# Kernel tuning notes

Measured on AMD Instinct MI355X. Metric: run time of the kernel, lower is better.

Reference implementation:

```python
import jax, jax.numpy as jnp
import numpy as np

B, L, D, H = 2, 2048, 2048, 16
DH = D // H  # 128 per-head dim
EPS = 1e-5


def setup_inputs() -> dict:
    key = jax.random.key(0)
    ks = jax.random.split(key, 6)
    s = 0.02  # xavier-ish init scale with gain 2**-2.5
    return {
        "hidden_states": jax.random.normal(ks[0], (B, L, D), jnp.float32),
        "Wq": jax.random.normal(ks[1], (D, D), jnp.float32) * s,
        "Wk": jax.random.normal(ks[2], (D, D), jnp.float32) * s,
        "Wv": jax.random.normal(ks[3], (D, D), jnp.float32) * s,
        "Wb": jax.random.normal(ks[4], (D, H), jnp.float32) * s,
        "o_norm_weight": jnp.ones((DH,), jnp.float32),
        "Wo": jax.random.normal(ks[5], (D, D), jnp.float32) * s,
    }


def _delta_rule(q, k, v, beta):
    """Recurrent delta-rule linear attention.
    q,k,v: [B,H,L,Dh]; beta: [B,H,L]. Math identical to fused_chunk_delta_rule.
    S_t = S_{t-1} + k_t (beta_t * (v_t - S_{t-1}^T k_t))^T ;  o_t = S_t^T q_t
    """
    def step(S, inp):
        qt, kt, vt, bt = inp  # [B,H,Dh],[B,H,Dh],[B,H,Dh],[B,H]
        v_pred = jnp.einsum('bhk,bhkv->bhv', kt, S)
        delta = (vt - v_pred) * bt[..., None]
        S = S + kt[..., None] * delta[:, :, None, :]
        ot = jnp.einsum('bhk,bhkv->bhv', qt, S)
        return S, ot

    xs = (q.transpose(2, 0, 1, 3), k.transpose(2, 0, 1, 3),
          v.transpose(2, 0, 1, 3), beta.transpose(2, 0, 1))
    S0 = jnp.zeros(q.shape[:2] + (q.shape[-1], v.shape[-1]), q.dtype)
    _, o = jax.lax.scan(step, S0, xs)  # o: [L,B,H,Dh]
    return o.transpose(1, 2, 0, 3)  # [B,H,L,Dh]


def reference(hidden_states, Wq, Wk, Wv, Wb, o_norm_weight, Wo):
    b, l, d = hidden_states.shape
    h = Wb.shape[1]
    dh = d // h

    q = hidden_states @ Wq
    k = hidden_states @ Wk
    v = jax.nn.silu(hidden_states @ Wv)

    def heads(x):
        return x.reshape(b, l, h, dh).transpose(0, 2, 1, 3)  # b h l d

    q, k, v = heads(q), heads(k), heads(v)

    # qk_norm = 'l2' (torch F.normalize with eps clamp)
    def l2n(x):
        n = jnp.sqrt(jnp.sum(x * x, axis=-1, keepdims=True))
        return x / jnp.maximum(n, 1e-12)

    q, k = l2n(q), l2n(k)
    q = q * (dh ** -0.5)  # fla delta-rule default scale

    beta = jax.nn.sigmoid(hidden_states @ Wb).transpose(0, 2, 1)  # b h l

    o = _delta_rule(q, k, v, beta)  # b h l dh
    o = o.transpose(0, 2, 1, 3)  # b l h dh

    # RMSNorm over head_v_dim
    o = o * jax.lax.rsqrt(jnp.mean(o * o, axis=-1, keepdims=True) + EPS)
    o = o * o_norm_weight

    return o.reshape(b, l, d) @ Wo
```

## Files before the change

kernel.cpp:

```cpp
#include <hip/hip_runtime.h>
#include <hip/hip_bf16.h>
#include <cstdint>

#define DEV static __device__ __forceinline__

typedef unsigned short u16;
typedef unsigned int u32;
typedef __attribute__((ext_vector_type(8))) short short8;
typedef __attribute__((ext_vector_type(4))) float f32x4;

constexpr int Bn = 2, Ln = 2048, Dn = 2048, Hn = 16;
constexpr int Mrows = Bn * Ln;
constexpr int CHK = 64, NCK = Ln / CHK;
constexpr int NCHUNKS = Bn * Hn * NCK;

DEV float b2f(u16 s) { union { float f; u32 u; } x; x.u = ((u32)s) << 16; return x.f; }
DEV u16 f2b(float f) {
  union { float f; u32 u; } x; x.f = f; u32 u = x.u;
  return (u16)((u + 0x7fffu + ((u >> 16) & 1u)) >> 16);
}

DEV void cp16(const void* g, void* l) {
  __builtin_amdgcn_global_load_lds(
      (const __attribute__((address_space(1))) u32*)(unsigned long long)(g),
      (__attribute__((address_space(3))) u32*)(unsigned long long)(l), 16, 0, 0);
}

DEV f32x4 mfma16(short8 a, short8 b, f32x4 c) {
  return __builtin_amdgcn_mfma_f32_16x16x32_bf16(a, b, c, 0, 0, 0);
}

__global__ void k_cvt(const float* __restrict__ src, u16* __restrict__ dst, int n8) {
  int i = blockIdx.x * blockDim.x + threadIdx.x;
  if (i >= n8) return;
  const float4* s4 = (const float4*)(src + (size_t)i * 8);
  float4 a = s4[0], b = s4[1];
  u16 o[8] = {f2b(a.x), f2b(a.y), f2b(a.z), f2b(a.w), f2b(b.x), f2b(b.y), f2b(b.z), f2b(b.w)};
  *(short8*)(dst + (size_t)i * 8) = *(short8*)o;
}

struct TransArgs {
  const float* src[5]; u16* dst[5]; int rows[5]; int cols[5];
};
__global__ void k_trans(TransArgs t) {
  __shared__ u16 tile[32][33];
  int z = blockIdx.z;
  const float* src = t.src[z]; u16* dst = t.dst[z];
  int rows = t.rows[z], cols = t.cols[z];
  int r0 = blockIdx.y * 32, c0 = blockIdx.x * 32;
  if (r0 >= rows || c0 >= cols) return;
  int tx = threadIdx.x, ty = threadIdx.y;
  for (int i = ty; i < 32; i += 8) {
    int r = r0 + i, c = c0 + tx;
    if (r < rows && c < cols) tile[i][tx] = f2b(src[(size_t)r * cols + c]);
  }
  __syncthreads();
  for (int i = ty; i < 32; i += 8) {
    int r = c0 + i, c = r0 + tx;
    if (r < cols && c < rows) dst[(size_t)r * rows + c] = tile[tx][i];
  }
}

__global__ __launch_bounds__(256) void k_beta(const u16* __restrict__ hs,
                                              const u16* __restrict__ WbT,
                                              float* __restrict__ beta_g) {
  __shared__ float part[256];
  int tid = threadIdx.x, wave = tid >> 6, lane = tid & 63, quad = lane >> 4, l15 = lane & 15;
  int tok0 = blockIdx.x * 16;
  const u16* arow = hs + (size_t)(tok0 + l15) * Dn + wave * 512;
  const u16* brow = WbT + (size_t)l15 * Dn + wave * 512;
  f32x4 acc = {0.f, 0.f, 0.f, 0.f};
#pragma unroll
  for (int k = 0; k < 512; k += 32) {
    short8 af = *(const short8*)&arow[k + quad * 8];
    short8 bf = *(const short8*)&brow[k + quad * 8];
    acc = mfma16(af, bf, acc);
  }
  part[tid] = 0.f;
  __syncthreads();
#pragma unroll
  for (int r = 0; r < 4; r++) atomicAdd(&part[l15 * 16 + quad * 4 + r], acc[r]);
  __syncthreads();
  int h = tid >> 4, tr = tid & 15;
  int b = tok0 >> 11;
  int l = (tok0 + tr) & 2047;
  beta_g[(size_t)(b * Hn + h) * Ln + l] = 1.f / (1.f + __expf(-part[h * 16 + tr]));
}

struct GemmArgs {
  const u16* A; const u16* Bt; void* C; int epi;
  int f32out;
  int M, N, K;
};
__global__ __launch_bounds__(256) void k_gemm(GemmArgs g) {
  __shared__ u16 As[128 * 64];
  __shared__ u16 Bs[128 * 64];
  const u16* A = g.A; const u16* Bt = g.Bt;
  int epi = g.epi;
  int K = g.K, N = g.N;
  int tid = threadIdx.x, wave = tid >> 6, lane = tid & 63;
  int quad = lane >> 4, l15 = lane & 15;
  int lin = blockIdx.y * gridDim.x + blockIdx.x;
  int cpx = (gridDim.x * gridDim.y) >> 3;
  int wg2 = (lin & 7) * cpx + (lin >> 3);
  int bx2 = wg2 % gridDim.x, by2 = wg2 / gridDim.x;
  int m0 = by2 * 128, n0 = bx2 * 128;
  int wm = (wave >> 1) * 64, wn = (wave & 1) * 64;
  f32x4 acc[4][4];
#pragma unroll
  for (int i = 0; i < 4; i++)
#pragma unroll
    for (int j = 0; j < 4; j++) acc[i][j] = (f32x4){0.f, 0.f, 0.f, 0.f};
  int scol = ((lane & 7) ^ (lane >> 3)) * 8;
  const u16* Ag = A + (size_t)(m0 + wave * 32 + (lane >> 3)) * K + scol;
  const u16* Bg = Bt + (size_t)(n0 + wave * 32 + (lane >> 3)) * K + scol;
  u16* Al = &As[wave * 32 * 64];
  u16* Bl = &Bs[wave * 32 * 64];
  int sw8 = l15 & 7;
  for (int k0 = 0; k0 < K; k0 += 64) {
#pragma unroll
    for (int t = 0; t < 4; t++) {
      cp16(Ag + k0 + t * 8 * K, Al + t * 8 * 64);
      cp16(Bg + k0 + t * 8 * K, Bl + t * 8 * 64);
    }
    __syncthreads();
#pragma unroll
    for (int kk = 0; kk < 64; kk += 32) {
      int sl = (((kk >> 3) + quad) ^ sw8) * 8;
      short8 af[4], bf[4];
#pragma unroll
      for (int i = 0; i < 4; i++) af[i] = *(const short8*)&As[(wm + i * 16 + l15) * 64 + sl];
#pragma unroll
      for (int i = 0; i < 4; i++) bf[i] = *(const short8*)&Bs[(wn + i * 16 + l15) * 64 + sl];
#pragma unroll
      for (int i = 0; i < 4; i++)
#pragma unroll
        for (int j = 0; j < 4; j++) acc[i][j] = mfma16(af[i], bf[j], acc[i][j]);
    }
    __syncthreads();
  }
#pragma unroll
  for (int i = 0; i < 4; i++)
#pragma unroll
    for (int j = 0; j < 4; j++) {
      int row = m0 + wm + i * 16 + quad * 4;
      int col = n0 + wn + j * 16 + l15;
#pragma unroll
      for (int r = 0; r < 4; r++) {
        float v = acc[i][j][r];
        if (epi == 1) v = v / (1.f + __expf(-v));
        if (g.f32out) ((float*)g.C)[(size_t)(row + r) * N + col] = v;
        else ((u16*)g.C)[(size_t)(row + r) * N + col] = f2b(v);
      }
    }
}

struct Gemm2Args { const u16* A; const u16* Bt; u16* C; int K; };

__global__ __launch_bounds__(512, 2) void k_gemm2(Gemm2Args g) {
  __shared__ u16 ldsbuf[61440];
  const char* LB = (const char*)ldsbuf;
  const int K = g.K, NT = K / 64;
  const size_t Kb = (size_t)K * 2;
  int tid = threadIdx.x, wave = tid >> 6, lane = tid & 63;
  int quad = lane >> 4, l15 = lane & 15;
  int wm = wave >> 2, wn = wave & 3;

  int bid = blockIdx.x;
  int wg = (bid & 7) * 32 + (bid >> 3);
  int by = wg >> 4, bx = wg & 15;
  int m0 = by * 256, n0f = bx * 384;

  int r0 = tid >> 2;
  int cby = (((tid & 3) ^ ((tid >> 3) & 3)) * 16);
  const char* gA = (const char*)g.A + (size_t)(m0 + r0) * Kb + cby;
  const char* gB = (const char*)g.Bt + (size_t)(n0f + r0) * Kb + cby;

  auto stageA = [&](int slot, int t, int kh) {
    const char* src = gA + (size_t)t * 128 + kh * 64;
    u16* dst = &ldsbuf[slot * 8192 + tid * 8];
    cp16(src, dst);
    cp16(src + (size_t)128 * Kb, dst + 4096);
  };
  auto stageB = [&](int slot, int t, int kh) {
    const char* src = gB + (size_t)t * 128 + kh * 64;
    u16* dst = &ldsbuf[24576 + slot * 12288 + tid * 8];
    cp16(src, dst);
    cp16(src + (size_t)128 * Kb, dst + 4096);
    cp16(src + (size_t)256 * Kb, dst + 8192);
  };

  f32x4 acc0[4][6], acc1[4][6];
#pragma unroll
  for (int i = 0; i < 4; i++)
#pragma unroll
    for (int j = 0; j < 6; j++) {
      acc0[i][j] = (f32x4){0.f, 0.f, 0.f, 0.f};
      acc1[i][j] = (f32x4){0.f, 0.f, 0.f, 0.f};
    }

  int rsw = (l15 >> 1) & 3;
  int rA = (wm * 128 + l15) * 64 + ((quad ^ rsw) * 16);
  int rB = (wn * 96 + l15) * 64 + ((quad ^ rsw) * 16);

  stageA(0, 0, 0);
  stageB(0, 0, 0);
  stageA(1, 0, 1);
  stageB(1, 0, 1);

  short8 bf[6];
  int u0 = 0;
  for (int t = 0; t < NT; ++t) {
    int u1 = u0 + 1; if (u1 == 3) u1 = 0;
    int u2 = u1 + 1; if (u2 == 3) u2 = 0;
    bool pf = (t + 1 < NT);
    const char* aK0 = LB + u0 * 16384;
    const char* aK1 = LB + u1 * 16384;
    const char* bK0 = LB + 49152 + u0 * 24576;
    const char* bK1 = LB + 49152 + u1 * 24576;

    asm volatile("s_waitcnt vmcnt(5)" ::: "memory");
    __builtin_amdgcn_s_barrier();
    __builtin_amdgcn_sched_barrier(0);
    if (pf) stageA(u2, t + 1, 0);
    {
      short8 av[4];
#pragma unroll
      for (int i = 0; i < 4; i++) av[i] = *(const short8*)(aK0 + rA + i * 1024);
#pragma unroll
      for (int j = 0; j < 6; j++) bf[j] = *(const short8*)(bK0 + rB + j * 1024);
      __builtin_amdgcn_s_setprio(1);
#pragma unroll
      for (int i = 0; i < 4; i++)
#pragma unroll
        for (int j = 0; j < 6; j++) acc0[i][j] = mfma16(av[i], bf[j], acc0[i][j]);
      __builtin_amdgcn_s_setprio(0);
    }

    asm volatile("s_waitcnt vmcnt(5)" ::: "memory");
    __builtin_amdgcn_s_barrier();
    __builtin_amdgcn_sched_barrier(0);
    if (pf) stageB(u2, t + 1, 0);
    {
      short8 av[4];
#pragma unroll
      for (int i = 0; i < 4; i++) av[i] = *(const short8*)(aK0 + rA + 4096 + i * 1024);
      __builtin_amdgcn_s_setprio(1);
#pragma unroll
      for (int i = 0; i < 4; i++)
#pragma unroll
        for (int j = 0; j < 6; j++) acc1[i][j] = mfma16(av[i], bf[j], acc1[i][j]);
      __builtin_amdgcn_s_setprio(0);
    }

    if (t == NT - 1) asm volatile("s_waitcnt vmcnt(0)" ::: "memory");
    else asm volatile("s_waitcnt vmcnt(5)" ::: "memory");
    __builtin_amdgcn_s_barrier();
    __builtin_amdgcn_sched_barrier(0);
    if (pf) stageA(u0, t + 1, 1);
    {
      short8 av[4];
#pragma unroll
      for (int i = 0; i < 4; i++) av[i] = *(const short8*)(aK1 + rA + i * 1024);
#pragma unroll
      for (int j = 0; j < 6; j++) bf[j] = *(const short8*)(bK1 + rB + j * 1024);
      __builtin_amdgcn_s_setprio(1);
#pragma unroll
      for (int i = 0; i < 4; i++)
#pragma unroll
        for (int j = 0; j < 6; j++) acc0[i][j] = mfma16(av[i], bf[j], acc0[i][j]);
      __builtin_amdgcn_s_setprio(0);
    }

    asm volatile("s_waitcnt vmcnt(5)" ::: "memory");
    __builtin_amdgcn_s_barrier();
    __builtin_amdgcn_sched_barrier(0);
    if (pf) stageB(u0, t + 1, 1);
    {
      short8 av[4];
#pragma unroll
      for (int i = 0; i < 4; i++) av[i] = *(const short8*)(aK1 + rA + 4096 + i * 1024);
      __builtin_amdgcn_s_setprio(1);
#pragma unroll
      for (int i = 0; i < 4; i++)
#pragma unroll
        for (int j = 0; j < 6; j++) acc1[i][j] = mfma16(av[i], bf[j], acc1[i][j]);
      __builtin_amdgcn_s_setprio(0);
    }

    u0 = u2;
  }

#pragma unroll
  for (int mq = 0; mq < 2; mq++) {
#pragma unroll
    for (int i = 0; i < 4; i++)
#pragma unroll
      for (int j = 0; j < 6; j++) {
        f32x4 a = mq ? acc1[i][j] : acc0[i][j];
        int row = m0 + wm * 128 + mq * 64 + i * 16 + quad * 4;
        int colg = n0f + wn * 96 + j * 16;
        int z = colg >> 11;
        u16* Cz = g.C + (size_t)z * ((size_t)Mrows * 2048);
        int col = (colg & 2047) + l15;
#pragma unroll
        for (int r = 0; r < 4; r++) {
          float v = a[r];
          if (z == 2) v = v / (1.f + __expf(-v));
          Cz[(size_t)(row + r) * 2048 + col] = f2b(v);
        }
      }
  }
}

__global__ void k_l2(u16* qn, u16* kn) {
  int tid = threadIdx.x, wave = tid >> 6, lane = tid & 63;
  size_t row = (size_t)blockIdx.x * 4 + wave;
  u16* p = (blockIdx.y ? kn : qn) + row * 128;
  u32 u = *(const u32*)&p[lane * 2];
  float x0 = b2f((u16)(u & 0xffff)), x1 = b2f((u16)(u >> 16));
  float ss = x0 * x0 + x1 * x1;
#pragma unroll
  for (int o = 32; o > 0; o >>= 1) ss += __shfl_xor(ss, o, 64);
  float sc = 1.f / fmaxf(sqrtf(ss), 1e-12f);
  if (blockIdx.y == 0) sc *= 0.08838834764831845f;
  u32 outv = (u32)f2b(x0 * sc) | ((u32)f2b(x1 * sc) << 16);
  *(u32*)&p[lane * 2] = outv;
}

constexpr int ST = 72;
__global__ __launch_bounds__(256, 4) void k_pre(
    const float* __restrict__ beta_g,
    const u16* __restrict__ qn, const u16* __restrict__ kn, const u16* __restrict__ vn,
    u16* __restrict__ W2g, u16* __restrict__ Ug, u16* __restrict__ Gg, u16* __restrict__ KTg) {
  __shared__ float beta_s[64];
  __shared__ u16 mats[4 * 64 * ST];
  int gid = blockIdx.x;
  int c = gid & 31, h = (gid >> 5) & 15, b = gid >> 9;
  int tid = threadIdx.x;
  int l0 = c * 64;

  if (tid < 64) beta_s[tid] = beta_g[(size_t)(b * Hn + h) * Ln + l0 + tid];
  __syncthreads();

  int wave = tid >> 6, lane = tid & 63, quad = lane >> 4, l15 = lane & 15;
  u16 *Br = mats, *Bc = mats + 64 * ST, *M0 = mats + 2 * 64 * ST, *M1 = mats + 3 * 64 * ST;

  {
    const u16* krowB = kn + (size_t)(b * Ln + l0 + wave * 16 + l15) * Dn + h * 128;
    short8 bfr[4];
#pragma unroll
    for (int s = 0; s < 4; s++) bfr[s] = *(const short8*)&krowB[quad * 8 + 32 * s];
#pragma unroll
    for (int mt = 0; mt < 4; ++mt) {
      const u16* arow_k = kn + (size_t)(b * Ln + l0 + mt * 16 + l15) * Dn + h * 128;
      const u16* arow_q = qn + (size_t)(b * Ln + l0 + mt * 16 + l15) * Dn + h * 128;
      f32x4 accA = {0.f, 0.f, 0.f, 0.f}, accG = {0.f, 0.f, 0.f, 0.f};
#pragma unroll
      for (int s = 0; s < 4; s++) {
        short8 ak = *(const short8*)&arow_k[quad * 8 + 32 * s];
        short8 aq = *(const short8*)&arow_q[quad * 8 + 32 * s];
        accA = mfma16(ak, bfr[s], accA);
        accG = mfma16(aq, bfr[s], accG);
      }
      int t = wave * 16 + l15;
#pragma unroll
      for (int r = 0; r < 4; r++) {
        int i = mt * 16 + quad * 4 + r;
        u16 nb = f2b((t < i) ? -beta_s[i] * accA[r] : 0.f);
        Br[i * ST + t] = nb;
        Bc[t * ST + i] = nb;
        M0[i * ST + t] = (t == i) ? f2b(1.f) : nb;
        Gg[(size_t)gid * 4096 + (size_t)i * 64 + t] = f2b((t <= i) ? accG[r] : 0.f);
      }
    }
  }
  __syncthreads();

  u16 *Mc = M0, *Mn = M1;
#pragma unroll
  for (int it = 0; it < 5; ++it) {
    const int tT = (it < 3) ? 0 : ((it == 3) ? 1 : 2);
    const int tI = (it < 4) ? 0 : 1;
    short8 bb[2];
#pragma unroll
    for (int s = 0; s < 2; s++) bb[s] = *(const short8*)&Bc[(wave * 16 + l15) * ST + quad * 8 + 32 * s];
    f32x4 accT[4];
#pragma unroll
    for (int mt = 0; mt < 4; mt++) {
      accT[mt] = (f32x4){0.f, 0.f, 0.f, 0.f};
      if (mt - wave >= tT) {
#pragma unroll
        for (int s = 0; s < 2; s++) {
          short8 af = *(const short8*)&Br[(mt * 16 + l15) * ST + quad * 8 + 32 * s];
          accT[mt] = mfma16(af, bb[s], accT[mt]);
        }
      }
    }
    __syncthreads();
#pragma unroll
    for (int mt = 0; mt < 4; mt++) {
      if (mt - wave >= tI) {
#pragma unroll
        for (int r = 0; r < 4; r++) {
          int i = mt * 16 + quad * 4 + r, t = wave * 16 + l15;
          u16 v = f2b(accT[mt][r]);
          Br[i * ST + t] = v;
          Bc[t * ST + i] = v;
        }
      }
    }
    __syncthreads();
    short8 tb[2];
#pragma unroll
    for (int s = 0; s < 2; s++) tb[s] = *(const short8*)&Bc[(wave * 16 + l15) * ST + quad * 8 + 32 * s];
#pragma unroll
    for (int mt = 0; mt < 4; mt++) {
      if (mt - wave >= tT) {
        f32x4 a;
#pragma unroll
        for (int r = 0; r < 4; r++) a[r] = b2f(Mc[(mt * 16 + quad * 4 + r) * ST + wave * 16 + l15]);
#pragma unroll
        for (int s = 0; s < 2; s++) {
          short8 af = *(const short8*)&Mc[(mt * 16 + l15) * ST + quad * 8 + 32 * s];
          a = mfma16(af, tb[s], a);
        }
#pragma unroll
        for (int r = 0; r < 4; r++) Mn[(mt * 16 + quad * 4 + r) * ST + wave * 16 + l15] = f2b(a[r]);
      } else {
#pragma unroll
        for (int r = 0; r < 4; r++)
          Mn[(mt * 16 + quad * 4 + r) * ST + wave * 16 + l15] =
              Mc[(mt * 16 + quad * 4 + r) * ST + wave * 16 + l15];
      }
    }
    u16* tmp = Mc; Mc = Mn; Mn = tmp;
  }
  __syncthreads();

  u16* XT = mats;
  for (int pass = 0; pass < 2; ++pass) {
    const u16* src = pass ? vn : kn;
    for (int idx = tid; idx < 64 * 128; idx += 256) {
      int t = idx >> 7, dk = idx & 127;
      float v = b2f(src[(size_t)(b * Ln + l0 + t) * Dn + h * 128 + dk]);
      XT[dk * ST + t] = f2b(v * beta_s[t]);
      if (pass == 0) KTg[(size_t)gid * 8192 + (size_t)dk * 64 + t] = f2b(v);
    }
    __syncthreads();
    u16* dst = pass ? Ug : W2g;
#pragma unroll
    for (int half = 0; half < 2; ++half) {
      int nt = wave + half * 4;
      short8 bx[2];
#pragma unroll
      for (int s = 0; s < 2; s++) bx[s] = *(const short8*)&XT[(nt * 16 + l15) * ST + quad * 8 + 32 * s];
#pragma unroll
      for (int mt = 0; mt < 4; mt++) {
        f32x4 a = {0.f, 0.f, 0.f, 0.f};
#pragma unroll
        for (int s = 0; s < 2; s++) {
          short8 af = *(const short8*)&Mc[(mt * 16 + l15) * ST + quad * 8 + 32 * s];
          a = mfma16(af, bx[s], a);
        }
#pragma unroll
        for (int r = 0; r < 4; r++)
          dst[(size_t)gid * 8192 + (size_t)(mt * 16 + quad * 4 + r) * 128 + nt * 16 + l15] = f2b(a[r]);
      }
    }
    __syncthreads();
  }
}

struct Frg { short8 w2[4], qf[4], gf[2], k0[2], k1[2]; float u[4]; };

__global__ __launch_bounds__(256) void k_scan(
    const u16* __restrict__ qn, const u16* __restrict__ W2g, const u16* __restrict__ Ug,
    const u16* __restrict__ Gg, const u16* __restrict__ KTg, u16* __restrict__ Og) {
  constexpr int SST = 136, DST = 104;
  __shared__ u16 Sb[16 * SST];
  __shared__ u16 Db[16 * DST];
  int bh = blockIdx.x, sl = blockIdx.y;
  int b = bh >> 4, h = bh & 15, c0 = sl * 16;
  int tid = threadIdx.x, wave = tid >> 6, lane = tid & 63, quad = lane >> 4, l15 = lane & 15;
  for (int i = tid; i < 16 * SST; i += 256) Sb[i] = 0;
  f32x4 accS0 = {0.f, 0.f, 0.f, 0.f}, accS1 = {0.f, 0.f, 0.f, 0.f};
  __syncthreads();

  auto load_frags = [&](Frg& F, int ci) {
    size_t ck = (size_t)bh * NCK + ci;
    const u16* w2row = W2g + ck * 8192 + (size_t)(wave * 16 + l15) * 128;
    const u16* qrow = qn + (size_t)(b * Ln + ci * 64 + wave * 16 + l15) * Dn + h * 128;
#pragma unroll
    for (int s = 0; s < 4; s++) {
      F.w2[s] = *(const short8*)&w2row[quad * 8 + 32 * s];
      F.qf[s] = *(const short8*)&qrow[quad * 8 + 32 * s];
    }
    const u16* grow = Gg + ck * 4096 + (size_t)(wave * 16 + l15) * 64;
    const u16* kt0 = KTg + ck * 8192 + (size_t)(wave * 16 + l15) * 64;
    const u16* kt1 = KTg + ck * 8192 + (size_t)((wave + 4) * 16 + l15) * 64;
#pragma unroll
    for (int s = 0; s < 2; s++) {
      F.gf[s] = *(const short8*)&grow[quad * 8 + 32 * s];
      F.k0[s] = *(const short8*)&kt0[quad * 8 + 32 * s];
      F.k1[s] = *(const short8*)&kt1[quad * 8 + 32 * s];
    }
    const u16* urow = Ug + ck * 8192 + (size_t)(wave * 16 + quad * 4) * 128 + c0 + l15;
#pragma unroll
    for (int r = 0; r < 4; r++) F.u[r] = b2f(urow[(size_t)r * 128]);
  };

  auto compute = [&](const Frg& F, int ci) {
    f32x4 accT = {0.f, 0.f, 0.f, 0.f}, accO = {0.f, 0.f, 0.f, 0.f};
#pragma unroll
    for (int s = 0; s < 4; s++) {
      short8 sf = *(const short8*)&Sb[l15 * SST + quad * 8 + 32 * s];
      accT = mfma16(F.w2[s], sf, accT);
      accO = mfma16(F.qf[s], sf, accO);
    }
#pragma unroll
    for (int r = 0; r < 4; r++) {
      float d = F.u[r] - accT[r];
      Db[l15 * DST + wave * 16 + quad * 4 + r] = f2b(d);
    }
    __syncthreads();
#pragma unroll
    for (int s = 0; s < 2; s++) {
      short8 df = *(const short8*)&Db[l15 * DST + quad * 8 + 32 * s];
      accO = mfma16(F.gf[s], df, accO);
      accS0 = mfma16(F.k0[s], df, accS0);
      accS1 = mfma16(F.k1[s], df, accS1);
    }
    u16* orow = Og + (size_t)(b * Ln + ci * 64 + wave * 16 + quad * 4) * Dn + h * 128 + c0 + l15;
#pragma unroll
    for (int r = 0; r < 4; r++) orow[(size_t)r * Dn] = f2b(accO[r]);
#pragma unroll
    for (int r = 0; r < 4; r++) {
      Sb[l15 * SST + wave * 16 + quad * 4 + r] = f2b(accS0[r]);
      Sb[l15 * SST + (wave + 4) * 16 + quad * 4 + r] = f2b(accS1[r]);
    }
    __syncthreads();
  };

  Frg FA, FB;
  load_frags(FA, 0);
  for (int ci = 0; ci < NCK; ci += 2) {
    load_frags(FB, ci + 1);
    compute(FA, ci);
    if (ci + 2 < NCK) load_frags(FA, ci + 2);
    compute(FB, ci + 1);
  }
}

__global__ void k_rms(const u16* __restrict__ Og, const float* __restrict__ w, u16* __restrict__ out) {
  int tid = threadIdx.x, wave = tid >> 6, lane = tid & 63;
  size_t row = (size_t)blockIdx.x * 4 + wave;
  const u16* p = Og + row * 128;
  u32 u = *(const u32*)&p[lane * 2];
  float x0 = b2f((u16)(u & 0xffff)), x1 = b2f((u16)(u >> 16));
  float ss = x0 * x0 + x1 * x1;
#pragma unroll
  for (int o = 32; o > 0; o >>= 1) ss += __shfl_xor(ss, o, 64);
  float sc = rsqrtf(ss * (1.f / 128.f) + 1e-5f);
  float w0 = w[lane * 2], w1 = w[lane * 2 + 1];
  u32 o2 = (u32)f2b(x0 * sc * w0) | ((u32)f2b(x1 * sc * w1) << 16);
  *(u32*)&out[row * 128 + lane * 2] = o2;
}

extern "C" void kernel_launch(void* const* d_in, const int* in_sizes, int n_in,
                              void* d_out, int out_size, void* d_ws, size_t ws_size,
                              hipStream_t stream) {
  (void)in_sizes; (void)n_in; (void)out_size; (void)ws_size;
  const float* hs_f = (const float*)d_in[0];
  const float* Wq = (const float*)d_in[1];
  const float* Wk = (const float*)d_in[2];
  const float* Wv = (const float*)d_in[3];
  const float* Wb = (const float*)d_in[4];
  const float* onw = (const float*)d_in[5];
  const float* Wo = (const float*)d_in[6];

  char* ws = (char*)d_ws;
  size_t off = 0;
  auto alloc = [&](size_t bytes) -> void* {
    void* p = ws + off;
    off += (bytes + 255) & ~(size_t)255;
    return p;
  };
  const size_t WB = (size_t)2048 * 2048 * 2;
  const size_t XB = (size_t)4096 * 2048 * 2;
  u16* WqT = (u16*)alloc(WB);
  u16* WkT = (u16*)alloc(WB);
  u16* WvT = (u16*)alloc(WB);
  u16* WoT = (u16*)alloc(WB);
  u16* WbT = (u16*)alloc((size_t)16 * 2048 * 2);
  u16* hsb = (u16*)alloc(XB);
  u16* qn  = (u16*)alloc(XB);
  u16* kn  = (u16*)alloc(XB);
  u16* vn  = (u16*)alloc(XB);
  u16* W2g = (u16*)alloc((size_t)NCHUNKS * 8192 * 2);
  u16* Ug  = (u16*)alloc((size_t)NCHUNKS * 8192 * 2);
  u16* Gg  = (u16*)alloc((size_t)NCHUNKS * 4096 * 2);
  u16* KTg = (u16*)alloc((size_t)NCHUNKS * 8192 * 2);
  float* beta_g = (float*)alloc((size_t)Bn * Hn * Ln * 4);
  u16* Og = vn;
  u16* onorm = qn;

  hipLaunchKernelGGL(k_cvt, dim3(Mrows * Dn / 8 / 256), dim3(256), 0, stream, hs_f, hsb, Mrows * Dn / 8);

  TransArgs ta;
  ta.src[0] = Wq; ta.dst[0] = WqT; ta.rows[0] = 2048; ta.cols[0] = 2048;
  ta.src[1] = Wk; ta.dst[1] = WkT; ta.rows[1] = 2048; ta.cols[1] = 2048;
  ta.src[2] = Wv; ta.dst[2] = WvT; ta.rows[2] = 2048; ta.cols[2] = 2048;
  ta.src[3] = Wo; ta.dst[3] = WoT; ta.rows[3] = 2048; ta.cols[3] = 2048;
  ta.src[4] = Wb; ta.dst[4] = WbT; ta.rows[4] = 2048; ta.cols[4] = 16;
  hipLaunchKernelGGL(k_trans, dim3(64, 64, 5), dim3(32, 8), 0, stream, ta);

  hipLaunchKernelGGL(k_beta, dim3(Mrows / 16), dim3(256), 0, stream, hsb, WbT, beta_g);

  {
    Gemm2Args g2;
    g2.A = hsb; g2.Bt = WqT; g2.C = qn; g2.K = 2048;
    hipLaunchKernelGGL(k_gemm2, dim3(256), dim3(512), 0, stream, g2);
  }

  hipLaunchKernelGGL(k_l2, dim3(16384, 2), dim3(256), 0, stream, qn, kn);

  hipLaunchKernelGGL(k_pre, dim3(NCHUNKS), dim3(256), 0, stream,
                     beta_g, qn, kn, vn, W2g, Ug, Gg, KTg);

  hipLaunchKernelGGL(k_scan, dim3(32, 8), dim3(256), 0, stream,
                     qn, W2g, Ug, Gg, KTg, Og);

  hipLaunchKernelGGL(k_rms, dim3(16384), dim3(256), 0, stream, Og, onw, onorm);

  GemmArgs go;
  go.A = onorm; go.Bt = WoT; go.C = d_out; go.epi = 0;
  go.f32out = 1; go.M = Mrows; go.N = 2048; go.K = 2048;
  hipLaunchKernelGGL(k_gemm, dim3(16, 32), dim3(256), 0, stream, go);
}
```

Before: 476.8 us.

## Replace output GEMM with pipelined triple-buffered kernel and vectorize chunk preprocessing loads

The simple 128x128 output-projection GEMM is replaced by a 512-thread, 128x256-tile kernel. It triple-buffers LDS via async global-to-LDS copies, waits on explicit vmcnt, and raises MFMA priority, so loads overlap compute. In k_pre, beta scaling moves from each loaded element onto the 64x64 transform matrix, and k/v tiles are loaded with 16-byte vector reads. The K transpose is also written to global from LDS as vectors instead of scattered scalar stores. The changes add hand-tuned wait counts and an extra bf16 rounding of the beta-scaled matrix, which slightly alters numerics.

After: 446.7 us. -6.3%, faster.

```diff
diff --git a/kernel.cpp b/kernel.cpp
--- a/kernel.cpp
+++ b/kernel.cpp
@@ -87,74 +87,6 @@
   beta_g[(size_t)(b * Hn + h) * Ln + l] = 1.f / (1.f + __expf(-part[h * 16 + tr]));
 }
 
-struct GemmArgs {
-  const u16* A; const u16* Bt; void* C; int epi;
-  int f32out;
-  int M, N, K;
-};
-__global__ __launch_bounds__(256) void k_gemm(GemmArgs g) {
-  __shared__ u16 As[128 * 64];
-  __shared__ u16 Bs[128 * 64];
-  const u16* A = g.A; const u16* Bt = g.Bt;
-  int epi = g.epi;
-  int K = g.K, N = g.N;
-  int tid = threadIdx.x, wave = tid >> 6, lane = tid & 63;
-  int quad = lane >> 4, l15 = lane & 15;
-  int lin = blockIdx.y * gridDim.x + blockIdx.x;
-  int cpx = (gridDim.x * gridDim.y) >> 3;
-  int wg2 = (lin & 7) * cpx + (lin >> 3);
-  int bx2 = wg2 % gridDim.x, by2 = wg2 / gridDim.x;
-  int m0 = by2 * 128, n0 = bx2 * 128;
-  int wm = (wave >> 1) * 64, wn = (wave & 1) * 64;
-  f32x4 acc[4][4];
-#pragma unroll
-  for (int i = 0; i < 4; i++)
-#pragma unroll
-    for (int j = 0; j < 4; j++) acc[i][j] = (f32x4){0.f, 0.f, 0.f, 0.f};
-  int scol = ((lane & 7) ^ (lane >> 3)) * 8;
-  const u16* Ag = A + (size_t)(m0 + wave * 32 + (lane >> 3)) * K + scol;
-  const u16* Bg = Bt + (size_t)(n0 + wave * 32 + (lane >> 3)) * K + scol;
-  u16* Al = &As[wave * 32 * 64];
-  u16* Bl = &Bs[wave * 32 * 64];
-  int sw8 = l15 & 7;
-  for (int k0 = 0; k0 < K; k0 += 64) {
-#pragma unroll
-    for (int t = 0; t < 4; t++) {
-      cp16(Ag + k0 + t * 8 * K, Al + t * 8 * 64);
-      cp16(Bg + k0 + t * 8 * K, Bl + t * 8 * 64);
-    }
-    __syncthreads();
-#pragma unroll
-    for (int kk = 0; kk < 64; kk += 32) {
-      int sl = (((kk >> 3) + quad) ^ sw8) * 8;
-      short8 af[4], bf[4];
-#pragma unroll
-      for (int i = 0; i < 4; i++) af[i] = *(const short8*)&As[(wm + i * 16 + l15) * 64 + sl];
-#pragma unroll
-      for (int i = 0; i < 4; i++) bf[i] = *(const short8*)&Bs[(wn + i * 16 + l15) * 64 + sl];
-#pragma unroll
-      for (int i = 0; i < 4; i++)
-#pragma unroll
-        for (int j = 0; j < 4; j++) acc[i][j] = mfma16(af[i], bf[j], acc[i][j]);
-    }
-    __syncthreads();
-  }
-#pragma unroll
-  for (int i = 0; i < 4; i++)
-#pragma unroll
-    for (int j = 0; j < 4; j++) {
-      int row = m0 + wm + i * 16 + quad * 4;
-      int col = n0 + wn + j * 16 + l15;
-#pragma unroll
-      for (int r = 0; r < 4; r++) {
-        float v = acc[i][j][r];
-        if (epi == 1) v = v / (1.f + __expf(-v));
-        if (g.f32out) ((float*)g.C)[(size_t)(row + r) * N + col] = v;
-        else ((u16*)g.C)[(size_t)(row + r) * N + col] = f2b(v);
-      }
-    }
-}
-
 struct Gemm2Args { const u16* A; const u16* Bt; u16* C; int K; };
 
 __global__ __launch_bounds__(512, 2) void k_gemm2(Gemm2Args g) {
@@ -313,6 +245,148 @@
   }
 }
 
+struct GemmoArgs { const u16* A; const u16* Bt; float* C; int K; };
+
+__global__ __launch_bounds__(512, 2) void k_gemmo(GemmoArgs g) {
+  __shared__ u16 ldsbuf[36864];
+  const char* LB = (const char*)ldsbuf;
+  const int K = g.K, NT = K / 64;
+  const size_t Kb = (size_t)K * 2;
+  int tid = threadIdx.x, wave = tid >> 6, lane = tid & 63;
+  int quad = lane >> 4, l15 = lane & 15;
+  int wm = wave >> 2, wn = wave & 3;
+
+  int bid = blockIdx.x;
+  int wg = (bid & 7) * 32 + (bid >> 3);
+  int bx = wg >> 5, by = wg & 31;
+  int m0 = by * 128, n0 = bx * 256;
+
+  int r0 = tid >> 2;
+  int cby = (((tid & 3) ^ ((tid >> 3) & 3)) * 16);
+  const char* gA = (const char*)g.A + (size_t)(m0 + r0) * Kb + cby;
+  const char* gB = (const char*)g.Bt + (size_t)(n0 + r0) * Kb + cby;
+
+  auto stageA = [&](int slot, int t, int kh) {
+    const char* src = gA + (size_t)t * 128 + kh * 64;
+    cp16(src, &ldsbuf[slot * 4096 + tid * 8]);
+  };
+  auto stageB = [&](int slot, int t, int kh) {
+    const char* src = gB + (size_t)t * 128 + kh * 64;
+    u16* dst = &ldsbuf[12288 + slot * 8192 + tid * 8];
+    cp16(src, dst);
+    cp16(src + (size_t)128 * Kb, dst + 4096);
+  };
+
+  f32x4 acc[4][4];
+#pragma unroll
+  for (int i = 0; i < 4; i++)
+#pragma unroll
+    for (int j = 0; j < 4; j++) acc[i][j] = (f32x4){0.f, 0.f, 0.f, 0.f};
+
+  int rsw = (l15 >> 1) & 3;
+  int rA = (wm * 64 + l15) * 64 + ((quad ^ rsw) * 16);
+  int rB = (wn * 64 + l15) * 64 + ((quad ^ rsw) * 16);
+
+  stageA(0, 0, 0);
+  stageB(0, 0, 0);
+  stageA(1, 0, 1);
+  stageB(1, 0, 1);
+
+  short8 av[4];
+  int u0 = 0;
+  for (int t = 0; t < NT; ++t) {
+    int u1 = u0 + 1; if (u1 == 3) u1 = 0;
+    int u2 = u1 + 1; if (u2 == 3) u2 = 0;
+    bool pf = (t + 1 < NT);
+    const char* aK0 = LB + u0 * 8192;
+    const char* aK1 = LB + u1 * 8192;
+    const char* bK0 = LB + 24576 + u0 * 16384;
+    const char* bK1 = LB + 24576 + u1 * 16384;
+
+    asm volatile("s_waitcnt vmcnt(3)" ::: "memory");
+    __builtin_amdgcn_s_barrier();
+    __builtin_amdgcn_sched_barrier(0);
+    if (pf) stageA(u2, t + 1, 0);
+    {
+      short8 bv[2];
+#pragma unroll
+      for (int i = 0; i < 4; i++) av[i] = *(const short8*)(aK0 + rA + i * 1024);
+#pragma unroll
+      for (int j = 0; j < 2; j++) bv[j] = *(const short8*)(bK0 + rB + j * 1024);
+      __builtin_amdgcn_s_setprio(1);
+#pragma unroll
+      for (int i = 0; i < 4; i++)
+#pragma unroll
+        for (int j = 0; j < 2; j++) acc[i][j] = mfma16(av[i], bv[j], acc[i][j]);
+      __builtin_amdgcn_s_setprio(0);
+    }
+
+    asm volatile("s_waitcnt vmcnt(3)" ::: "memory");
+    __builtin_amdgcn_s_barrier();
+    __builtin_amdgcn_sched_barrier(0);
+    if (pf) stageB(u2, t + 1, 0);
+    {
+      short8 bv[2];
+#pragma unroll
+      for (int j = 0; j < 2; j++) bv[j] = *(const short8*)(bK0 + rB + (2 + j) * 1024);
+      __builtin_amdgcn_s_setprio(1);
+#pragma unroll
+      for (int i = 0; i < 4; i++)
+#pragma unroll
+        for (int j = 0; j < 2; j++) acc[i][2 + j] = mfma16(av[i], bv[j], acc[i][2 + j]);
+      __builtin_amdgcn_s_setprio(0);
+    }
+
+    if (t == NT - 1) asm volatile("s_waitcnt vmcnt(0)" ::: "memory");
+    else asm volatile("s_waitcnt vmcnt(3)" ::: "memory");
+    __builtin_amdgcn_s_barrier();
+    __builtin_amdgcn_sched_barrier(0);
+    if (pf) stageA(u0, t + 1, 1);
+    {
+      short8 bv[2];
+#pragma unroll
+      for (int i = 0; i < 4; i++) av[i] = *(const short8*)(aK1 + rA + i * 1024);
+#pragma unroll
+      for (int j = 0; j < 2; j++) bv[j] = *(const short8*)(bK1 + rB + j * 1024);
+      __builtin_amdgcn_s_setprio(1);
+#pragma unroll
+      for (int i = 0; i < 4; i++)
+#pragma unroll
+        for (int j = 0; j < 2; j++) acc[i][j] = mfma16(av[i], bv[j], acc[i][j]);
+      __builtin_amdgcn_s_setprio(0);
+    }
+
+    asm volatile("s_waitcnt vmcnt(3)" ::: "memory");
+    __builtin_amdgcn_s_barrier();
+    __builtin_amdgcn_sched_barrier(0);
+    if (pf) stageB(u0, t + 1, 1);
+    {
+      short8 bv[2];
+#pragma unroll
+      for (int j = 0; j < 2; j++) bv[j] = *(const short8*)(bK1 + rB + (2 + j) * 1024);
+      __builtin_amdgcn_s_setprio(1);
+#pragma unroll
+      for (int i = 0; i < 4; i++)
+#pragma unroll
+        for (int j = 0; j < 2; j++) acc[i][2 + j] = mfma16(av[i], bv[j], acc[i][2 + j]);
+      __builtin_amdgcn_s_setprio(0);
+    }
+
+    u0 = u2;
+  }
+
+#pragma unroll
+  for (int i = 0; i < 4; i++)
+#pragma unroll
+    for (int j = 0; j < 4; j++) {
+      int row = m0 + wm * 64 + i * 16 + quad * 4;
+      int col = n0 + wn * 64 + j * 16 + l15;
+#pragma unroll
+      for (int r = 0; r < 4; r++)
+        g.C[(size_t)(row + r) * 2048 + col] = acc[i][j][r];
+    }
+}
+
 __global__ void k_l2(u16* qn, u16* kn) {
   int tid = threadIdx.x, wave = tid >> 6, lane = tid & 63;
   size_t row = (size_t)blockIdx.x * 4 + wave;
@@ -439,15 +513,35 @@
   __syncthreads();
 
   u16* XT = mats;
+  u16* Mb = Mn;
+  for (int idx = tid; idx < 512; idx += 256) {
+    int i = idx >> 3, t8 = (idx & 7) * 8;
+    short8 m8 = *(const short8*)&Mc[i * ST + t8];
+    short8 o8;
+#pragma unroll
+    for (int e = 0; e < 8; e++) o8[e] = (short)f2b(b2f((u16)m8[e]) * beta_s[t8 + e]);
+    *(short8*)&Mb[i * ST + t8] = o8;
+  }
+  int tv = tid & 63, dk0 = (tid >> 6) * 32;
   for (int pass = 0; pass < 2; ++pass) {
     const u16* src = pass ? vn : kn;
-    for (int idx = tid; idx < 64 * 128; idx += 256) {
-      int t = idx >> 7, dk = idx & 127;
-      float v = b2f(src[(size_t)(b * Ln + l0 + t) * Dn + h * 128 + dk]);
-      XT[dk * ST + t] = f2b(v * beta_s[t]);
-      if (pass == 0) KTg[(size_t)gid * 8192 + (size_t)dk * 64 + t] = f2b(v);
+    const u16* srow = src + (size_t)(b * Ln + l0 + tv) * Dn + h * 128 + dk0;
+#pragma unroll
+    for (int s = 0; s < 4; s++) {
+      short8 vv = *(const short8*)&srow[s * 8];
+#pragma unroll
+      for (int e = 0; e < 8; e++) XT[(dk0 + s * 8 + e) * ST + tv] = (u16)vv[e];
     }
     __syncthreads();
+    if (pass == 0) {
+#pragma unroll
+      for (int it2 = 0; it2 < 4; it2++) {
+        int idx = tid + it2 * 256;
+        int dk = idx >> 3, t0 = (idx & 7) * 8;
+        *(short8*)&KTg[(size_t)gid * 8192 + dk * 64 + t0] =
+            *(const short8*)&XT[dk * ST + t0];
+      }
+    }
     u16* dst = pass ? Ug : W2g;
 #pragma unroll
     for (int half = 0; half < 2; ++half) {
@@ -460,7 +554,7 @@
         f32x4 a = {0.f, 0.f, 0.f, 0.f};
 #pragma unroll
         for (int s = 0; s < 2; s++) {
-          short8 af = *(const short8*)&Mc[(mt * 16 + l15) * ST + quad * 8 + 32 * s];
+          short8 af = *(const short8*)&Mb[(mt * 16 + l15) * ST + quad * 8 + 32 * s];
           a = mfma16(af, bx[s], a);
         }
 #pragma unroll
@@ -633,8 +727,9 @@
 
   hipLaunchKernelGGL(k_rms, dim3(16384), dim3(256), 0, stream, Og, onw, onorm);
 
-  GemmArgs go;
-  go.A = onorm; go.Bt = WoT; go.C = d_out; go.epi = 0;
-  go.f32out = 1; go.M = Mrows; go.N = 2048; go.K = 2048;
-  hipLaunchKernelGGL(k_gemm, dim3(16, 32), dim3(256), 0, stream, go);
-}
+  {
+    GemmoArgs go;
+    go.A = onorm; go.Bt = WoT; go.C = (float*)d_out; go.K = 2048;
+    hipLaunchKernelGGL(k_gemmo, dim3(256), dim3(512), 0, stream, go);
+  }
+}
```
